# Kernel optimization log

Measured on AMD Instinct MI355X. Metric: run time of the kernel, lower is better.

Reference implementation:

```python
import jax, jax.numpy as jnp
import numpy as np

K = 32  # num_nearest_neighbors

def silu(x):
    return x * jax.nn.sigmoid(x)

def setup_inputs() -> dict:
    key = jax.random.key(0)
    ks = jax.random.split(key, 10)
    b, n, d, m = 4, 2048, 64, 16
    e_in = 2 * d + 1  # 129 = fourier*2 + dim*2 + edge_dim + 1
    std = 0.001  # init_eps normal init on Linear weights
    inp = {
        "feats": jax.random.normal(ks[0], (b, n, d), dtype=jnp.float32),
        "coors": jax.random.normal(ks[1], (b, n, 3), dtype=jnp.float32),
        # edge_mlp: Linear(129,258) -> SiLU -> Linear(258,16) -> SiLU
        "ew1": jax.random.normal(ks[2], (e_in, 2 * e_in), dtype=jnp.float32) * std,
        "eb1": jnp.zeros((2 * e_in,), dtype=jnp.float32),
        "ew2": jax.random.normal(ks[3], (2 * e_in, m), dtype=jnp.float32) * std,
        "eb2": jnp.zeros((m,), dtype=jnp.float32),
        # coors_mlp: Linear(16,64) -> SiLU -> Linear(64,1)
        "cw1": jax.random.normal(ks[4], (m, 4 * m), dtype=jnp.float32) * std,
        "cb1": jnp.zeros((4 * m,), dtype=jnp.float32),
        "cw2": jax.random.normal(ks[5], (4 * m, 1), dtype=jnp.float32) * std,
        "cb2": jnp.zeros((1,), dtype=jnp.float32),
        # node_mlp: Linear(80,128) -> SiLU -> Linear(128,64)
        "nw1": jax.random.normal(ks[6], (d + m, 2 * d), dtype=jnp.float32) * std,
        "nb1": jnp.zeros((2 * d,), dtype=jnp.float32),
        "nw2": jax.random.normal(ks[7], (2 * d, d), dtype=jnp.float32) * std,
        "nb2": jnp.zeros((d,), dtype=jnp.float32),
    }
    return inp


def reference(feats, coors, ew1, eb1, ew2, eb2, cw1, cb1, cw2, cb2, nw1, nb1, nw2, nb2):
    b, n, d = feats.shape
    # pairwise relative coords / squared distances: [b,n,n,3], [b,n,n]
    rel = coors[:, :, None, :] - coors[:, None, :, :]
    dist2 = jnp.sum(rel * rel, axis=-1)
    # k nearest neighbors (smallest squared distance)
    _, idx = jax.lax.top_k(-dist2, K)  # idx: [b,n,K]
    bi = jnp.arange(b)[:, None, None]
    ii = jnp.arange(n)[None, :, None]
    rel_k = rel[bi, ii, idx]                # [b,n,K,3]
    dist_k = dist2[bi, ii, idx][..., None]  # [b,n,K,1]
    feats_j = feats[bi, idx]                # [b,n,K,d]
    feats_i = jnp.broadcast_to(feats[:, :, None, :], feats_j.shape)
    # edge MLP
    edge_in = jnp.concatenate([feats_i, feats_j, dist_k], axis=-1)  # [b,n,K,2d+1]
    h = silu(edge_in @ ew1 + eb1)
    m_ij = silu(h @ ew2 + eb2)  # [b,n,K,m]
    # coordinate update
    coor_w = (silu(m_ij @ cw1 + cb1) @ cw2 + cb2)[..., 0]  # [b,n,K]
    coors_out = jnp.einsum('bik,bikc->bic', coor_w, rel_k) + coors
    # node update (sum pooling over neighbors)
    m_i = jnp.sum(m_ij, axis=-2)  # [b,n,m]
    node_in = jnp.concatenate([feats, m_i], axis=-1)
    node_out = silu(node_in @ nw1 + nb1) @ nw2 + nb2 + feats
    return (node_out, coors_out)
```

## Files before the change

### kernel.cpp

```cpp
#include <hip/hip_runtime.h>
#include <math.h>

#define NB 4
#define NN 2048
#define ND 64
#define NM 16
#define NK 32
#define EIN 129
#define EH 258
#define CHD 64
#define NHD 128
#define PQS 288
#define XS 96
#define KNN_BLOCKS (NB * NN / 4)
#define PREP_BLOCKS 92

typedef __attribute__((ext_vector_type(8))) short short8;
typedef __attribute__((ext_vector_type(4))) float f32x4;
typedef __attribute__((ext_vector_type(4))) int intx4;

__device__ __forceinline__ float fast_silu(float x) {
    return x * __builtin_amdgcn_rcpf(1.f + __expf(-x));
}

__device__ __forceinline__ short f2bf(float f) {
    union { float f; unsigned u; } v; v.f = f;
    unsigned r = v.u + 0x7FFFu + ((v.u >> 16) & 1u);
    return (short)(r >> 16);
}

__device__ __forceinline__ float bf2f(short s) {
    union { unsigned u; float f; } v;
    v.u = ((unsigned)(unsigned short)s) << 16;
    return v.f;
}

__device__ __forceinline__ unsigned cvt_pk_bf16(float lo, float hi) {
    unsigned r;
    asm("v_cvt_pk_bf16_f32 %0, %1, %2" : "=v"(r) : "v"(lo), "v"(hi));
    return r;
}

__device__ __forceinline__ unsigned umin_u(unsigned a, unsigned b) { return a < b ? a : b; }
__device__ __forceinline__ unsigned umax_u(unsigned a, unsigned b) { return a > b ? a : b; }

__global__ __launch_bounds__(256) void pk_kernel(
    const float* __restrict__ coors, int* __restrict__ idx_out,
    const float* __restrict__ ew1, const float* __restrict__ ew2, const float* __restrict__ eb1,
    const float* __restrict__ cw1,
    const float* __restrict__ nw1, const float* __restrict__ nw2,
    float* __restrict__ w1pad, float* __restrict__ eb1pad,
    short* __restrict__ W2T, short* __restrict__ W1F, short* __restrict__ cw1T,
    short* __restrict__ nw1F, short* __restrict__ nw2F) {
    __shared__ union {
        float clds[NN * 3];
        unsigned slds[4][NN];
    } sm;
    const int tid = threadIdx.x;

    if (blockIdx.x >= KNN_BLOCKS) {
        const int blk = blockIdx.x - KNN_BLOCKS;
        if (blk < 72) {
            const int kk = blk & 1, ct = (blk >> 1) % 18, half = blk / 36;
            for (int t = tid; t < 512; t += 256) {
                const int l = t >> 3, i = t & 7;
                const int er = l & 15, grp = l >> 4;
                const int k = kk * 32 + grp * 8 + i;
                const int col = ct * 16 + er;
                const int row = half * 64 + k;
                W1F[blk * 512 + t] = (col < EH) ? f2bf(ew1[row * EH + col]) : (short)0;
            }
        } else if (blk == 72) {
            for (int c = tid; c < PQS; c += 256) {
                w1pad[c] = (c < EH) ? ew1[128 * EH + c] : 0.f;
                eb1pad[c] = (c < EH) ? eb1[c] : 0.f;
            }
        } else if (blk < 89) {
            const int t = blk - 73;
            for (int k = tid; k < PQS; k += 256)
                W2T[t * PQS + k] = (k < EH) ? f2bf(ew2[k * NM + t]) : (short)0;
        } else if (blk == 89) {
            for (int t2 = tid; t2 < CHD * NM; t2 += 256) {
                const int h = t2 >> 4, t = t2 & 15;
                cw1T[t2] = f2bf(cw1[t * CHD + h]);
            }
        } else if (blk == 90) {
            for (int t = tid; t < 24 * 512; t += 256) {
                const int f = t >> 9, t2 = t & 511;
                const int ct = f / 3, kk = f % 3;
                const int l = t2 >> 3, i = t2 & 7;
                const int er = l & 15, grp = l >> 4;
                const int k = kk * 32 + grp * 8 + i;
                const int col = ct * 16 + er;
                nw1F[t] = (k < 80) ? f2bf(nw1[k * NHD + col]) : (short)0;
            }
        } else {
            for (int t = tid; t < 16 * 512; t += 256) {
                const int f = t >> 9, t2 = t & 511;
                const int ct = f >> 2, kk = f & 3;
                const int l = t2 >> 3, i = t2 & 7;
                const int er = l & 15, grp = l >> 4;
                const int k = kk * 32 + grp * 8 + i;
                const int col = ct * 16 + er;
                nw2F[t] = f2bf(nw2[k * ND + col]);
            }
        }
        return;
    }

    const int wv = tid >> 6;
    const int lane = tid & 63;
    const int row0 = blockIdx.x * 4;
    const int b = row0 >> 11;
    const float* cb = coors + (size_t)b * NN * 3;
    for (int t = tid; t < NN * 3; t += 256) sm.clds[t] = cb[t];
    __syncthreads();

    const int row = row0 + wv;
    const int i = row & (NN - 1);
    const float cix = sm.clds[i * 3 + 0], ciy = sm.clds[i * 3 + 1], ciz = sm.clds[i * 3 + 2];

    unsigned k[32];
    #pragma unroll
    for (int t = 0; t < 32; ++t) {
        int j = lane + 64 * t;
        float dx = cix - sm.clds[j * 3 + 0];
        float dy = ciy - sm.clds[j * 3 + 1];
        float dz = ciz - sm.clds[j * 3 + 2];
        float d = dx * dx + dy * dy + dz * dz;
        union { float f; unsigned u; } v; v.f = d;
        k[t] = (v.u & 0xFFFFF800u) | (unsigned)j;
    }
    __syncthreads();

    #pragma unroll
    for (int size = 2; size <= 32; size <<= 1) {
        #pragma unroll
        for (int stride = size >> 1; stride > 0; stride >>= 1) {
            #pragma unroll
            for (int t = 0; t < 32; ++t) {
                int p = t ^ stride;
                if (p > t) {
                    const bool up = ((t & size) == 0);
                    unsigned lo = umin_u(k[t], k[p]);
                    unsigned hi = umax_u(k[t], k[p]);
                    k[t] = up ? lo : hi;
                    k[p] = up ? hi : lo;
                }
            }
        }
    }
    #pragma unroll
    for (int t = 0; t < 32; ++t) sm.slds[wv][t * 64 + lane] = k[t];

    unsigned cur = k[0];
    int head = 0;
    int myidx = 0;
    for (int it = 0; it < NK; ++it) {
        unsigned w = cur;
        #pragma unroll
        for (int off = 1; off < 64; off <<= 1) {
            unsigned o = __shfl_xor(w, off);
            w = umin_u(w, o);
        }
        if (lane == it) myidx = (int)(w & 2047u);
        if (cur == w) {
            ++head;
            cur = (head < 32) ? sm.slds[wv][head * 64 + lane] : 0xFFFFFFFFu;
        }
    }
    if (lane < NK) idx_out[row * NK + lane] = myidx;
}

__global__ __launch_bounds__(256) void pq_kernel(const float* __restrict__ feats,
                                                 const short* __restrict__ W1F,
                                                 const float* __restrict__ eb1pad,
                                                 short* __restrict__ P,
                                                 short* __restrict__ Q,
                                                 short* __restrict__ xbuf) {
    const int wv = threadIdx.x >> 6, lane = threadIdx.x & 63;
    const int er = lane & 15, grp = lane >> 4;
    const int wid = blockIdx.x * 4 + wv;
    const int mt = wid / 18, ct = wid % 18;
    const int nb = mt * 16;

    short8 a[2];
    #pragma unroll
    for (int kk = 0; kk < 2; ++kk) {
        const float* fp = feats + (size_t)(nb + er) * ND + kk * 32 + grp * 8;
        f32x4 f0 = *(const f32x4*)fp;
        f32x4 f1 = *(const f32x4*)(fp + 4);
        union { intx4 iv; short8 s; } u;
        u.iv[0] = cvt_pk_bf16(f0[0], f0[1]);
        u.iv[1] = cvt_pk_bf16(f0[2], f0[3]);
        u.iv[2] = cvt_pk_bf16(f1[0], f1[1]);
        u.iv[3] = cvt_pk_bf16(f1[2], f1[3]);
        a[kk] = u.s;
    }

    if (ct == 0) {
        short* xr = xbuf + (size_t)(nb + er) * XS;
        *(short8*)(xr + 0 * 32 + grp * 8) = a[0];
        *(short8*)(xr + 1 * 32 + grp * 8) = a[1];
        if (grp == 0) {
            const short8 z8 = {0, 0, 0, 0, 0, 0, 0, 0};
            *(short8*)(xr + 80) = z8;
            *(short8*)(xr + 88) = z8;
        }
    }

    const short8* WF = (const short8*)W1F;
    short8 bP0 = WF[((0 * 18 + ct) * 2 + 0) * 64 + lane];
    short8 bP1 = WF[((0 * 18 + ct) * 2 + 1) * 64 + lane];
    short8 bQ0 = WF[((1 * 18 + ct) * 2 + 0) * 64 + lane];
    short8 bQ1 = WF[((1 * 18 + ct) * 2 + 1) * 64 + lane];

    f32x4 accP = {0.f, 0.f, 0.f, 0.f};
    f32x4 accQ = {0.f, 0.f, 0.f, 0.f};
    accP = __builtin_amdgcn_mfma_f32_16x16x32_bf16(a[0], bP0, accP, 0, 0, 0);
    accP = __builtin_amdgcn_mfma_f32_16x16x32_bf16(a[1], bP1, accP, 0, 0, 0);
    accQ = __builtin_amdgcn_mfma_f32_16x16x32_bf16(a[0], bQ0, accQ, 0, 0, 0);
    accQ = __builtin_amdgcn_mfma_f32_16x16x32_bf16(a[1], bQ1, accQ, 0, 0, 0);

    const float bias = eb1pad[ct * 16 + er];
    #pragma unroll
    for (int r = 0; r < 4; ++r) {
        const int node = nb + grp * 4 + r;
        P[(size_t)node * PQS + ct * 16 + er] = f2bf(accP[r] + bias);
        Q[(size_t)node * PQS + ct * 16 + er] = f2bf(accQ[r]);
    }
}

__global__ __launch_bounds__(256) void edge_kernel(
    const float* __restrict__ coors, const int* __restrict__ idx,
    const short* __restrict__ P, const short* __restrict__ Q,
    const float* __restrict__ w1pad, const short* __restrict__ W2T,
    const float* __restrict__ eb2,
    const short* __restrict__ cw1T, const float* __restrict__ cb1,
    const float* __restrict__ cw2, const float* __restrict__ cb2,
    float* __restrict__ coors_out, short* __restrict__ xbuf) {

    __shared__ __align__(16) short mtl[4][NK][NM];

    const int tid = threadIdx.x;
    const int wv = tid >> 6, lane = tid & 63;
    const int er = lane & 15, grp = lane >> 4;
    const int gi = blockIdx.x * 4 + wv;
    const int b = gi >> 11;

    const int j0 = idx[gi * NK + er];
    const int j1 = idx[gi * NK + 16 + er];
    const float ci0 = coors[gi * 3 + 0], ci1 = coors[gi * 3 + 1], ci2 = coors[gi * 3 + 2];
    const float* cj0p = coors + (size_t)(b * NN + j0) * 3;
    const float* cj1p = coors + (size_t)(b * NN + j1) * 3;
    const float r0x = ci0 - cj0p[0], r0y = ci1 - cj0p[1], r0z = ci2 - cj0p[2];
    const float r1x = ci0 - cj1p[0], r1y = ci1 - cj1p[1], r1z = ci2 - cj1p[2];
    const float d0 = r0x * r0x + r0y * r0y + r0z * r0z;
    const float d1 = r1x * r1x + r1y * r1y + r1z * r1z;

    const short8* Pr8 = (const short8*)(P + (size_t)gi * PQS);
    const short8* Q0 = (const short8*)(Q + (size_t)(b * NN + j0) * PQS);
    const short8* Q1 = (const short8*)(Q + (size_t)(b * NN + j1) * PQS);
    const short8* w2row = (const short8*)(W2T + er * PQS);
    const f32x4* w14 = (const f32x4*)w1pad;

    f32x4 acc0 = {0.f, 0.f, 0.f, 0.f};
    f32x4 acc1 = {0.f, 0.f, 0.f, 0.f};
    #pragma unroll
    for (int kk = 0; kk < 9; ++kk) {
        short8 bf = w2row[kk * 4 + grp];
        short8 pb = Pr8[kk * 4 + grp];
        short8 qb0 = Q0[kk * 4 + grp];
        short8 qb1 = Q1[kk * 4 + grp];
        f32x4 w0 = w14[kk * 8 + grp * 2];
        f32x4 w1 = w14[kk * 8 + grp * 2 + 1];
        float wf[8] = {w0[0], w0[1], w0[2], w0[3], w1[0], w1[1], w1[2], w1[3]};
        float pf[8];
        #pragma unroll
        for (int i = 0; i < 8; ++i) pf[i] = bf2f(pb[i]);
        float h0[8], h1[8];
        #pragma unroll
        for (int i = 0; i < 8; ++i) {
            h0[i] = fast_silu(fmaf(d0, wf[i], pf[i]) + bf2f(qb0[i]));
            h1[i] = fast_silu(fmaf(d1, wf[i], pf[i]) + bf2f(qb1[i]));
        }
        union { intx4 iv; short8 s; } u0, u1;
        u0.iv[0] = cvt_pk_bf16(h0[0], h0[1]);
        u0.iv[1] = cvt_pk_bf16(h0[2], h0[3]);
        u0.iv[2] = cvt_pk_bf16(h0[4], h0[5]);
        u0.iv[3] = cvt_pk_bf16(h0[6], h0[7]);
        u1.iv[0] = cvt_pk_bf16(h1[0], h1[1]);
        u1.iv[1] = cvt_pk_bf16(h1[2], h1[3]);
        u1.iv[2] = cvt_pk_bf16(h1[4], h1[5]);
        u1.iv[3] = cvt_pk_bf16(h1[6], h1[7]);
        acc0 = __builtin_amdgcn_mfma_f32_16x16x32_bf16(u0.s, bf, acc0, 0, 0, 0);
        acc1 = __builtin_amdgcn_mfma_f32_16x16x32_bf16(u1.s, bf, acc1, 0, 0, 0);
    }

    const float eb2v = eb2[er];
    float m0[4], m1[4];
    #pragma unroll
    for (int r = 0; r < 4; ++r) {
        m0[r] = fast_silu(acc0[r] + eb2v);
        m1[r] = fast_silu(acc1[r] + eb2v);
    }

    float s = m0[0] + m0[1] + m0[2] + m0[3] + m1[0] + m1[1] + m1[2] + m1[3];
    s += __shfl_xor(s, 16);
    s += __shfl_xor(s, 32);
    if (lane < NM) xbuf[(size_t)gi * XS + ND + er] = f2bf(s);

    #pragma unroll
    for (int r = 0; r < 4; ++r) {
        mtl[wv][grp * 4 + r][er] = f2bf(m0[r]);
        mtl[wv][16 + grp * 4 + r][er] = f2bf(m1[r]);
    }
    __syncthreads();

    const short8 zero8 = {0, 0, 0, 0, 0, 0, 0, 0};
    short8 afr[4];
    #pragma unroll
    for (int mt = 0; mt < 4; ++mt)
        afr[mt] = (grp < 2) ? *(const short8*)(cw1T + (mt * 16 + er) * NM + grp * 8) : zero8;

    float cwv[2];
    #pragma unroll
    for (int nt = 0; nt < 2; ++nt) {
        short8 bfr = (grp < 2) ? *(const short8*)&mtl[wv][nt * 16 + er][grp * 8] : zero8;
        float partial = 0.f;
        #pragma unroll
        for (int mt = 0; mt < 4; ++mt) {
            f32x4 dz = {0.f, 0.f, 0.f, 0.f};
            dz = __builtin_amdgcn_mfma_f32_16x16x32_bf16(afr[mt], bfr, dz, 0, 0, 0);
            f32x4 cb1v = *(const f32x4*)(cb1 + mt * 16 + grp * 4);
            f32x4 cw2v = *(const f32x4*)(cw2 + mt * 16 + grp * 4);
            #pragma unroll
            for (int r = 0; r < 4; ++r)
                partial += fast_silu(dz[r] + cb1v[r]) * cw2v[r];
        }
        partial += __shfl_xor(partial, 16);
        partial += __shfl_xor(partial, 32);
        cwv[nt] = partial + cb2[0];
    }

    float wx = cwv[0] * r0x + cwv[1] * r1x;
    float wy = cwv[0] * r0y + cwv[1] * r1y;
    float wz = cwv[0] * r0z + cwv[1] * r1z;
    #pragma unroll
    for (int off = 1; off < 16; off <<= 1) {
        wx += __shfl_xor(wx, off);
        wy += __shfl_xor(wy, off);
        wz += __shfl_xor(wz, off);
    }
    if (lane == 0) {
        coors_out[gi * 3 + 0] = ci0 + wx;
        coors_out[gi * 3 + 1] = ci1 + wy;
        coors_out[gi * 3 + 2] = ci2 + wz;
    }
}

__global__ __launch_bounds__(256) void node_kernel(
    const short* __restrict__ xbuf,
    const short* __restrict__ nw1F, const float* __restrict__ nb1,
    const short* __restrict__ nw2F, const float* __restrict__ nb2,
    const float* __restrict__ feats, float* __restrict__ node_out) {
    __shared__ __align__(16) short hl[16 * 128];
    const int tid = threadIdx.x;
    const int wv = tid >> 6, lane = tid & 63;
    const int er = lane & 15, grp = lane >> 4;
    const int nb = blockIdx.x * 16;

    short8 a[3];
    #pragma unroll
    for (int kk = 0; kk < 3; ++kk)
        a[kk] = *(const short8*)(xbuf + (size_t)(nb + er) * XS + kk * 32 + grp * 8);

    #pragma unroll
    for (int c2 = 0; c2 < 2; ++c2) {
        const int ct = wv * 2 + c2;
        f32x4 acc = {0.f, 0.f, 0.f, 0.f};
        #pragma unroll
        for (int kk = 0; kk < 3; ++kk)
            acc = __builtin_amdgcn_mfma_f32_16x16x32_bf16(
                a[kk], *(const short8*)(nw1F + (ct * 3 + kk) * 512 + lane * 8), acc, 0, 0, 0);
        const float b1 = nb1[ct * 16 + er];
        #pragma unroll
        for (int r = 0; r < 4; ++r) {
            const int row = grp * 4 + r;
            int byte = row * 256 + (ct * 16 + er) * 2;
            byte ^= (row & 7) << 4;
            *(short*)((char*)hl + byte) = f2bf(fast_silu(acc[r] + b1));
        }
    }
    __syncthreads();

    short8 a2[4];
    #pragma unroll
    for (int kk = 0; kk < 4; ++kk) {
        int byte = er * 256 + kk * 64 + grp * 16;
        byte ^= (er & 7) << 4;
        a2[kk] = *(const short8*)((const char*)hl + byte);
    }
    f32x4 acc = {0.f, 0.f, 0.f, 0.f};
    #pragma unroll
    for (int kk = 0; kk < 4; ++kk)
        acc = __builtin_amdgcn_mfma_f32_16x16x32_bf16(
            a2[kk], *(const short8*)(nw2F + (wv * 4 + kk) * 512 + lane * 8), acc, 0, 0, 0);
    const float b2 = nb2[wv * 16 + er];
    #pragma unroll
    for (int r = 0; r < 4; ++r) {
        const int node = nb + grp * 4 + r;
        node_out[(size_t)node * ND + wv * 16 + er] =
            acc[r] + b2 + feats[(size_t)node * ND + wv * 16 + er];
    }
}

extern "C" void kernel_launch(void* const* d_in, const int* in_sizes, int n_in,
                              void* d_out, int out_size, void* d_ws, size_t ws_size,
                              hipStream_t stream) {
    const float* feats = (const float*)d_in[0];
    const float* coors = (const float*)d_in[1];
    const float* ew1 = (const float*)d_in[2];
    const float* eb1 = (const float*)d_in[3];
    const float* ew2 = (const float*)d_in[4];
    const float* eb2 = (const float*)d_in[5];
    const float* cw1 = (const float*)d_in[6];
    const float* cb1 = (const float*)d_in[7];
    const float* cw2 = (const float*)d_in[8];
    const float* cb2 = (const float*)d_in[9];
    const float* nw1 = (const float*)d_in[10];
    const float* nb1 = (const float*)d_in[11];
    const float* nw2 = (const float*)d_in[12];
    const float* nb2 = (const float*)d_in[13];

    float* out_node = (float*)d_out;
    float* out_coors = out_node + (size_t)NB * NN * ND;

    char* ws = (char*)d_ws;
    int*   idx    = (int*)(ws + 0);
    short* P      = (short*)(ws + 1048576);
    short* Q      = (short*)(ws + 5767168);
    float* w1pad  = (float*)(ws + 10485760);
    float* eb1pad = (float*)(ws + 10486912);
    short* W2T    = (short*)(ws + 10488064);
    short* W1F    = (short*)(ws + 10497280);
    short* cw1T   = (short*)(ws + 10571008);
    short* nw1F   = (short*)(ws + 10573056);
    short* nw2F   = (short*)(ws + 10597632);
    short* xbuf   = (short*)(ws + 10614016);

    pk_kernel<<<KNN_BLOCKS + PREP_BLOCKS, 256, 0, stream>>>(
        coors, idx, ew1, ew2, eb1, cw1, nw1, nw2,
        w1pad, eb1pad, W2T, W1F, cw1T, nw1F, nw2F);
    pq_kernel<<<(512 * 18) / 4, 256, 0, stream>>>(feats, W1F, eb1pad, P, Q, xbuf);
    edge_kernel<<<NB * NN / 4, 256, 0, stream>>>(
        coors, idx, P, Q, w1pad, W2T, eb2, cw1T, cb1, cw2, cb2,
        out_coors, xbuf);
    node_kernel<<<NB * NN / 16, 256, 0, stream>>>(
        xbuf, nw1F, nb1, nw2F, nb2, feats, out_node);
}
```

Measured before the change: 92.65 us.

## Drop LDS staging in kNN, register-shift merge, swizzle blocks, prefetch Q rows

The kNN path stops staging all coordinates and the sorted key lists in shared memory. Each lane now reads neighbour coordinates directly from global memory (relying on cache), and the 32-way merge shifts a register array instead of reading heads back from LDS. Block indices in both the kNN and edge kernels are swizzled so consecutive blocks spread across batch/XCD groups, and the edge kernel issues all Q-row gathers up front to overlap their latency. The trade is more global loads and a 31-element conditional register shift per iteration, plus higher register pressure, in exchange for removing LDS usage and barriers and gaining occupancy and overlap.

```diff
diff --git a/kernel.cpp b/kernel.cpp
--- a/kernel.cpp
+++ b/kernel.cpp
@@ -52,10 +52,6 @@
     float* __restrict__ w1pad, float* __restrict__ eb1pad,
     short* __restrict__ W2T, short* __restrict__ W1F, short* __restrict__ cw1T,
     short* __restrict__ nw1F, short* __restrict__ nw2F) {
-    __shared__ union {
-        float clds[NN * 3];
-        unsigned slds[4][NN];
-    } sm;
     const int tid = threadIdx.x;
 
     if (blockIdx.x >= KNN_BLOCKS) {
@@ -108,30 +104,27 @@
         return;
     }
 
+    const int wg = ((blockIdx.x & 7) << 8) | (blockIdx.x >> 3);
     const int wv = tid >> 6;
     const int lane = tid & 63;
-    const int row0 = blockIdx.x * 4;
-    const int b = row0 >> 11;
+    const int row = wg * 4 + wv;
+    const int b = row >> 11;
+    const int i = row & (NN - 1);
     const float* cb = coors + (size_t)b * NN * 3;
-    for (int t = tid; t < NN * 3; t += 256) sm.clds[t] = cb[t];
-    __syncthreads();
-
-    const int row = row0 + wv;
-    const int i = row & (NN - 1);
-    const float cix = sm.clds[i * 3 + 0], ciy = sm.clds[i * 3 + 1], ciz = sm.clds[i * 3 + 2];
+    const float cix = cb[i * 3 + 0], ciy = cb[i * 3 + 1], ciz = cb[i * 3 + 2];
 
     unsigned k[32];
     #pragma unroll
     for (int t = 0; t < 32; ++t) {
         int j = lane + 64 * t;
-        float dx = cix - sm.clds[j * 3 + 0];
-        float dy = ciy - sm.clds[j * 3 + 1];
-        float dz = ciz - sm.clds[j * 3 + 2];
+        const float* cj = cb + (size_t)j * 3;
+        float dx = cix - cj[0];
+        float dy = ciy - cj[1];
+        float dz = ciz - cj[2];
         float d = dx * dx + dy * dy + dz * dz;
         union { float f; unsigned u; } v; v.f = d;
         k[t] = (v.u & 0xFFFFF800u) | (unsigned)j;
     }
-    __syncthreads();
 
     #pragma unroll
     for (int size = 2; size <= 32; size <<= 1) {
@@ -150,24 +143,20 @@
             }
         }
     }
-    #pragma unroll
-    for (int t = 0; t < 32; ++t) sm.slds[wv][t * 64 + lane] = k[t];
-
-    unsigned cur = k[0];
-    int head = 0;
+
     int myidx = 0;
     for (int it = 0; it < NK; ++it) {
-        unsigned w = cur;
+        unsigned w = k[0];
         #pragma unroll
         for (int off = 1; off < 64; off <<= 1) {
             unsigned o = __shfl_xor(w, off);
             w = umin_u(w, o);
         }
         if (lane == it) myidx = (int)(w & 2047u);
-        if (cur == w) {
-            ++head;
-            cur = (head < 32) ? sm.slds[wv][head * 64 + lane] : 0xFFFFFFFFu;
-        }
+        const bool won = (k[0] == w);
+        #pragma unroll
+        for (int t = 0; t < 31; ++t) k[t] = won ? k[t + 1] : k[t];
+        k[31] = won ? 0xFFFFFFFFu : k[31];
     }
     if (lane < NK) idx_out[row * NK + lane] = myidx;
 }
@@ -243,9 +232,10 @@
     __shared__ __align__(16) short mtl[4][NK][NM];
 
     const int tid = threadIdx.x;
+    const int wg = ((blockIdx.x & 7) << 8) | (blockIdx.x >> 3);
     const int wv = tid >> 6, lane = tid & 63;
     const int er = lane & 15, grp = lane >> 4;
-    const int gi = blockIdx.x * 4 + wv;
+    const int gi = wg * 4 + wv;
     const int b = gi >> 11;
 
     const int j0 = idx[gi * NK + er];
@@ -264,14 +254,19 @@
     const short8* w2row = (const short8*)(W2T + er * PQS);
     const f32x4* w14 = (const f32x4*)w1pad;
 
+    short8 qb0a[9], qb1a[9];
+    #pragma unroll
+    for (int kk = 0; kk < 9; ++kk) {
+        qb0a[kk] = Q0[kk * 4 + grp];
+        qb1a[kk] = Q1[kk * 4 + grp];
+    }
+
     f32x4 acc0 = {0.f, 0.f, 0.f, 0.f};
     f32x4 acc1 = {0.f, 0.f, 0.f, 0.f};
     #pragma unroll
     for (int kk = 0; kk < 9; ++kk) {
         short8 bf = w2row[kk * 4 + grp];
         short8 pb = Pr8[kk * 4 + grp];
-        short8 qb0 = Q0[kk * 4 + grp];
-        short8 qb1 = Q1[kk * 4 + grp];
         f32x4 w0 = w14[kk * 8 + grp * 2];
         f32x4 w1 = w14[kk * 8 + grp * 2 + 1];
         float wf[8] = {w0[0], w0[1], w0[2], w0[3], w1[0], w1[1], w1[2], w1[3]};
@@ -281,8 +276,8 @@
         float h0[8], h1[8];
         #pragma unroll
         for (int i = 0; i < 8; ++i) {
-            h0[i] = fast_silu(fmaf(d0, wf[i], pf[i]) + bf2f(qb0[i]));
-            h1[i] = fast_silu(fmaf(d1, wf[i], pf[i]) + bf2f(qb1[i]));
+            h0[i] = fast_silu(fmaf(d0, wf[i], pf[i]) + bf2f(qb0a[kk][i]));
+            h1[i] = fast_silu(fmaf(d1, wf[i], pf[i]) + bf2f(qb1a[kk][i]));
         }
         union { intx4 iv; short8 s; } u0, u1;
         u0.iv[0] = cvt_pk_bf16(h0[0], h0[1]);
```

Measured after the change: 108.3 us. 16.9% more time.
